# Kernel tuning notes

Measured on AMD Instinct MI355X. Metric: run time of the kernel, lower is better.

Reference implementation:

```python
import jax, jax.numpy as jnp
import numpy as np

N = 50000
E = 800000
IN_FEATS = 128
OUT_FEATS = 16
EDGE_FEATS = 1
NUM_HEADS = 8


def setup_inputs() -> dict:
    key = jax.random.key(0)
    ks = jax.random.split(key, 8)

    def xavier(k, shape):
        fan_in, fan_out = shape[-1], shape[-2] if len(shape) > 1 else shape[-1]
        bound = float(np.sqrt(6.0 / (shape[0] + shape[1])))
        return jax.random.uniform(k, shape, jnp.float32, -bound, bound)

    h = jax.random.normal(ks[0], (N, IN_FEATS), jnp.float32)
    edge_index = jax.random.randint(ks[1], (2, E), 0, N, jnp.int32)
    edge_feat = jax.random.normal(ks[2], (E, EDGE_FEATS), jnp.float32)
    # W_node stored as [in_feats, out_feats*num_heads] so h @ W_node == torch Linear(h)
    W_node = xavier(ks[3], (IN_FEATS, OUT_FEATS * NUM_HEADS))
    W_edge = xavier(ks[4], (EDGE_FEATS, NUM_HEADS))
    a_src = xavier(ks[5], (NUM_HEADS, OUT_FEATS))
    a_dst = xavier(ks[6], (NUM_HEADS, OUT_FEATS))
    return {"h": h, "edge_index": edge_index, "edge_feat": edge_feat,
            "W_node": W_node, "W_edge": W_edge, "a_src": a_src, "a_dst": a_dst}


def reference(h, edge_index, edge_feat, W_node, W_edge, a_src, a_dst):
    n = h.shape[0]
    src, dst = edge_index[0], edge_index[1]
    # node projection: [N, H, F]
    h_trans = (h @ W_node).reshape(n, NUM_HEADS, OUT_FEATS)
    # edge projection: [E, H]
    e_trans = edge_feat @ W_edge
    src_feat = h_trans[src]  # [E, H, F]
    dst_feat = h_trans[dst]  # [E, H, F]
    attn = (src_feat * a_src).sum(-1) + (dst_feat * a_dst).sum(-1) + e_trans  # [E, H]
    attn = jax.nn.leaky_relu(attn, negative_slope=0.2)
    # segment softmax over edges grouped by dst
    max_val = jax.ops.segment_max(attn, dst, num_segments=n)  # [N, H]
    exp_attn = jnp.exp(attn - max_val[dst])
    sum_exp = jax.ops.segment_sum(exp_attn, dst, num_segments=n)  # [N, H]
    alpha = exp_attn / jnp.maximum(sum_exp[dst], 1e-12)  # [E, H]
    msg = src_feat * alpha[..., None]  # [E, H, F]
    out = jax.ops.segment_sum(msg, dst, num_segments=n)  # [N, H, F]
    return out.mean(axis=1)  # [N, F]
```

## Files before the change

### kernel.cpp

```cpp
#include <hip/hip_runtime.h>

#define N_NODES 50000
#define N_EDGES 800000
#define IN_F    128
#define HEADS   8
#define OUT_F   16

typedef unsigned short u16;
typedef __attribute__((ext_vector_type(8))) short bf16x8;
typedef __attribute__((ext_vector_type(4))) float f32x4;

__device__ __forceinline__ float bf2f(u16 u) {
    return __uint_as_float(((unsigned)u) << 16);
}
__device__ __forceinline__ u16 f2bf(float f) {
    unsigned u = __float_as_uint(f);
    unsigned r = 0x7fffu + ((u >> 16) & 1u);
    return (u16)((u + r) >> 16);
}
__device__ __forceinline__ float ldf(const void* p, int i, bool bf) {
    return bf ? bf2f(((const u16*)p)[i]) : ((const float*)p)[i];
}

__global__ void probe_dtype(const void* __restrict__ h, int* __restrict__ flag) {
    if (threadIdx.x == 0 && blockIdx.x == 0) {
        const u16* u = (const u16*)h;
        int cnt = 0;
        for (int i = 0; i < 128; ++i) {
            int e = (u[i] >> 7) & 0xFF;
            if (e >= 90 && e <= 141) cnt++;
        }
        *flag = (cnt >= 110) ? 1 : 0;
    }
}

__global__ __launch_bounds__(256) void init_bufs(float* __restrict__ sum_exp,
                                                 float* __restrict__ out_acc) {
    int i = blockIdx.x * 256 + threadIdx.x;
    if (i < N_NODES * HEADS)  sum_exp[i] = 0.0f;
    if (i < N_NODES * OUT_F)  out_acc[i] = 0.0f;
}

#define WT_STRIDE 136
__global__ __launch_bounds__(256) void node_proj_mfma(
    const void* __restrict__ h, const void* __restrict__ Wn,
    const void* __restrict__ a_srcp, const void* __restrict__ a_dstp,
    const int* __restrict__ flag,
    u16* __restrict__ ht, float* __restrict__ s_src, float* __restrict__ s_dst)
{
    const bool bf = (*flag) != 0;
    __shared__ u16 Wsh[IN_F * WT_STRIDE];
    const int tid = threadIdx.x;

    for (int i = tid; i < IN_F * IN_F; i += 256) {
        int k = i >> 7, c = i & 127;
        u16 v = bf ? ((const u16*)Wn)[i] : f2bf(((const float*)Wn)[i]);
        Wsh[c * WT_STRIDE + k] = v;
    }
    __syncthreads();

    const int wave = tid >> 6, lane = tid & 63;
    const int m = lane & 15, q = lane >> 4;
    const int row_t = blockIdx.x * 64 + wave * 16;

    bf16x8 afr[4];
    int arow = row_t + m;
    if (arow >= N_NODES) arow = N_NODES - 1;
    if (bf) {
        const u16* hp = (const u16*)h + (size_t)arow * IN_F;
        #pragma unroll
        for (int kt = 0; kt < 4; ++kt)
            afr[kt] = *(const bf16x8*)(hp + kt * 32 + q * 8);
    } else {
        const float* hp = (const float*)h + (size_t)arow * IN_F;
        #pragma unroll
        for (int kt = 0; kt < 4; ++kt) {
            bf16x8 t;
            #pragma unroll
            for (int j = 0; j < 8; ++j) t[j] = (short)f2bf(hp[kt * 32 + q * 8 + j]);
            afr[kt] = t;
        }
    }

    for (int ct = 0; ct < 8; ++ct) {
        f32x4 acc = {0.f, 0.f, 0.f, 0.f};
        #pragma unroll
        for (int kt = 0; kt < 4; ++kt) {
            bf16x8 bfr = *(const bf16x8*)(Wsh + (ct * 16 + m) * WT_STRIDE + kt * 32 + q * 8);
            acc = __builtin_amdgcn_mfma_f32_16x16x32_bf16(afr[kt], bfr, acc, 0, 0, 0);
        }
        const float asv = ldf(a_srcp, ct * 16 + m, bf);
        const float adv = ldf(a_dstp, ct * 16 + m, bf);
        float v1[4], v2[4];
        #pragma unroll
        for (int r = 0; r < 4; ++r) {
            int grow = row_t + q * 4 + r;
            if (grow < N_NODES)
                ht[(size_t)grow * IN_F + ct * 16 + m] = f2bf(acc[r]);
            v1[r] = acc[r] * asv;
            v2[r] = acc[r] * adv;
        }
        #pragma unroll
        for (int o = 1; o < 16; o <<= 1) {
            #pragma unroll
            for (int r = 0; r < 4; ++r) {
                v1[r] += __shfl_xor(v1[r], o, 16);
                v2[r] += __shfl_xor(v2[r], o, 16);
            }
        }
        if (m == 0) {
            #pragma unroll
            for (int r = 0; r < 4; ++r) {
                int grow = row_t + q * 4 + r;
                if (grow < N_NODES) {
                    s_src[grow * HEADS + ct] = v1[r];
                    s_dst[grow * HEADS + ct] = v2[r];
                }
            }
        }
    }
}

__device__ __forceinline__ float edge_attn(const int* ei, const void* ef,
                                           const void* We,
                                           const float* s_src, const float* s_dst,
                                           int e, int hh, bool bf,
                                           int& src, int& dst) {
    src = ei[e];
    dst = ei[N_EDGES + e];
    float a = s_src[src * HEADS + hh] + s_dst[dst * HEADS + hh]
            + ldf(ef, e, bf) * ldf(We, hh, bf);
    return (a > 0.0f) ? a : 0.2f * a;
}

__global__ __launch_bounds__(256) void edge_sum(
    const int* __restrict__ ei, const void* __restrict__ ef,
    const void* __restrict__ We, const int* __restrict__ flag,
    const float* __restrict__ s_src, const float* __restrict__ s_dst,
    float* __restrict__ sum_exp)
{
    const bool bf = (*flag) != 0;
    int t = blockIdx.x * 256 + threadIdx.x;
    if (t >= N_EDGES * HEADS) return;
    int e = t >> 3, hh = t & 7, src, dst;
    float a = edge_attn(ei, ef, We, s_src, s_dst, e, hh, bf, src, dst);
    atomicAdd(&sum_exp[dst * HEADS + hh], __expf(a));
}

__global__ __launch_bounds__(256) void edge_aggregate(
    const int* __restrict__ ei, const void* __restrict__ ef,
    const void* __restrict__ We, const int* __restrict__ flag,
    const float* __restrict__ s_src, const float* __restrict__ s_dst,
    const float* __restrict__ sum_exp,
    const u16* __restrict__ ht, float* __restrict__ out_acc)
{
    const bool bf = (*flag) != 0;
    int t = blockIdx.x * 256 + threadIdx.x;
    int e = t >> 4;
    if (e >= N_EDGES) return;
    int lane = threadIdx.x & 15;
    int hh = lane & 7, src, dst;
    float a = edge_attn(ei, ef, We, s_src, s_dst, e, hh, bf, src, dst);
    float alpha = __expf(a) / fmaxf(sum_exp[dst * HEADS + hh], 1e-12f);

    const u16* hp = ht + (size_t)src * IN_F + lane;
    float acc = 0.0f;
    #pragma unroll
    for (int h2 = 0; h2 < HEADS; ++h2) {
        float ah = __shfl(alpha, h2, 16);
        acc = fmaf(ah, bf2f(hp[h2 * 16]), acc);
    }
    atomicAdd(&out_acc[dst * OUT_F + lane], acc * 0.125f);
}

__global__ __launch_bounds__(256) void finalize(const float* __restrict__ out_acc,
                                                void* __restrict__ out,
                                                const int* __restrict__ flag) {
    const bool bf = (*flag) != 0;
    int i = blockIdx.x * 256 + threadIdx.x;
    if (i < N_NODES * OUT_F) {
        float v = out_acc[i];
        if (bf) ((u16*)out)[i] = f2bf(v);
        else    ((float*)out)[i] = v;
    }
}

extern "C" void kernel_launch(void* const* d_in, const int* in_sizes, int n_in,
                              void* d_out, int out_size, void* d_ws, size_t ws_size,
                              hipStream_t stream) {
    const void* h     = d_in[0];
    const int*  ei    = (const int*)d_in[1];
    const void* efeat = d_in[2];
    const void* Wn    = d_in[3];
    const void* We    = d_in[4];
    const void* a_src = d_in[5];
    const void* a_dst = d_in[6];

    char* ws = (char*)d_ws;
    int*   flag    = (int*)ws;   ws += 256;
    u16*   ht      = (u16*)ws;   ws += (size_t)N_NODES * IN_F * 2;
    float* s_src   = (float*)ws; ws += (size_t)N_NODES * HEADS * 4;
    float* s_dst   = (float*)ws; ws += (size_t)N_NODES * HEADS * 4;
    float* sum_exp = (float*)ws; ws += (size_t)N_NODES * HEADS * 4;
    float* out_acc = (float*)ws; ws += (size_t)N_NODES * OUT_F * 4;

    hipLaunchKernelGGL(probe_dtype, dim3(1), dim3(64), 0, stream, h, flag);
    hipLaunchKernelGGL(init_bufs, dim3((N_NODES * OUT_F + 255) / 256), dim3(256),
                       0, stream, sum_exp, out_acc);
    hipLaunchKernelGGL(node_proj_mfma, dim3((N_NODES + 63) / 64), dim3(256),
                       0, stream, h, Wn, a_src, a_dst, flag, ht, s_src, s_dst);
    hipLaunchKernelGGL(edge_sum, dim3((N_EDGES * HEADS + 255) / 256), dim3(256),
                       0, stream, ei, efeat, We, flag, s_src, s_dst, sum_exp);
    hipLaunchKernelGGL(edge_aggregate, dim3((N_EDGES * 16 + 255) / 256), dim3(256),
                       0, stream, ei, efeat, We, flag, s_src, s_dst, sum_exp,
                       ht, out_acc);
    hipLaunchKernelGGL(finalize, dim3((N_NODES * OUT_F + 255) / 256), dim3(256),
                       0, stream, out_acc, d_out, flag);
}
```

Measured before the change: 225.7 us.

## Replace atomic edge softmax with CSR-by-destination segmented aggregation

Builds a CSR grouping of edges by destination (histogram, single-block scan, atomic scatter of src and edge features), then runs one 16-lane group per node. Each group computes the softmax weights, normalises them and accumulates messages in registers, with no max subtraction, which matches the earlier code. This removes the float atomics on sum_exp and out_acc, the second pass over edges and the finalize kernel. In exchange it adds a serial single-block scan, a scatter pass, load imbalance from per-node degree loops, and an edge order within each node that depends on the order of the scatter atomics.

```diff
diff --git a/kernel.cpp b/kernel.cpp
--- a/kernel.cpp
+++ b/kernel.cpp
@@ -34,11 +34,9 @@
     }
 }
 
-__global__ __launch_bounds__(256) void init_bufs(float* __restrict__ sum_exp,
-                                                 float* __restrict__ out_acc) {
+__global__ __launch_bounds__(256) void zero_counts(int* __restrict__ counts) {
     int i = blockIdx.x * 256 + threadIdx.x;
-    if (i < N_NODES * HEADS)  sum_exp[i] = 0.0f;
-    if (i < N_NODES * OUT_F)  out_acc[i] = 0.0f;
+    if (i < N_NODES) counts[i] = 0;
 }
 
 #define WT_STRIDE 136
@@ -121,67 +119,125 @@
     }
 }
 
-__device__ __forceinline__ float edge_attn(const int* ei, const void* ef,
-                                           const void* We,
-                                           const float* s_src, const float* s_dst,
-                                           int e, int hh, bool bf,
-                                           int& src, int& dst) {
-    src = ei[e];
-    dst = ei[N_EDGES + e];
-    float a = s_src[src * HEADS + hh] + s_dst[dst * HEADS + hh]
-            + ldf(ef, e, bf) * ldf(We, hh, bf);
-    return (a > 0.0f) ? a : 0.2f * a;
-}
-
-__global__ __launch_bounds__(256) void edge_sum(
+__global__ __launch_bounds__(256) void hist_dst(const int* __restrict__ ei,
+                                                int* __restrict__ counts) {
+    int t = blockIdx.x * 256 + threadIdx.x;
+    if (t < N_EDGES) atomicAdd(&counts[ei[N_EDGES + t]], 1);
+}
+
+#define SCAN_T 1024
+#define SCAN_C 49
+__global__ __launch_bounds__(SCAN_T) void scan_offsets(
+    const int* __restrict__ counts,
+    int* __restrict__ seg_off, int* __restrict__ cursor)
+{
+    __shared__ int partial[SCAN_T];
+    const int t = threadIdx.x;
+    const int base = t * SCAN_C;
+    int s = 0;
+    for (int j = 0; j < SCAN_C; ++j) {
+        int i = base + j;
+        if (i < N_NODES) s += counts[i];
+    }
+    partial[t] = s;
+    __syncthreads();
+    for (int o = 1; o < SCAN_T; o <<= 1) {
+        int v = (t >= o) ? partial[t - o] : 0;
+        __syncthreads();
+        if (t >= o) partial[t] += v;
+        __syncthreads();
+    }
+    int run = (t > 0) ? partial[t - 1] : 0;
+    for (int j = 0; j < SCAN_C; ++j) {
+        int i = base + j;
+        if (i < N_NODES) {
+            seg_off[i] = run;
+            cursor[i]  = run;
+            run += counts[i];
+        }
+    }
+}
+
+__global__ __launch_bounds__(256) void scatter_edges(
     const int* __restrict__ ei, const void* __restrict__ ef,
+    const int* __restrict__ flag, int* __restrict__ cursor,
+    int* __restrict__ src_s, float* __restrict__ ef_s)
+{
+    const bool bf = (*flag) != 0;
+    int t = blockIdx.x * 256 + threadIdx.x;
+    if (t >= N_EDGES) return;
+    int s = ei[t], d = ei[N_EDGES + t];
+    int pos = atomicAdd(&cursor[d], 1);
+    src_s[pos] = s;
+    ef_s[pos]  = ldf(ef, t, bf);
+}
+
+__global__ __launch_bounds__(256) void aggregate(
+    const int* __restrict__ seg_off, const int* __restrict__ counts,
+    const int* __restrict__ src_s, const float* __restrict__ ef_s,
     const void* __restrict__ We, const int* __restrict__ flag,
     const float* __restrict__ s_src, const float* __restrict__ s_dst,
-    float* __restrict__ sum_exp)
+    const u16* __restrict__ ht, void* __restrict__ out)
 {
     const bool bf = (*flag) != 0;
-    int t = blockIdx.x * 256 + threadIdx.x;
-    if (t >= N_EDGES * HEADS) return;
-    int e = t >> 3, hh = t & 7, src, dst;
-    float a = edge_attn(ei, ef, We, s_src, s_dst, e, hh, bf, src, dst);
-    atomicAdd(&sum_exp[dst * HEADS + hh], __expf(a));
-}
-
-__global__ __launch_bounds__(256) void edge_aggregate(
-    const int* __restrict__ ei, const void* __restrict__ ef,
-    const void* __restrict__ We, const int* __restrict__ flag,
-    const float* __restrict__ s_src, const float* __restrict__ s_dst,
-    const float* __restrict__ sum_exp,
-    const u16* __restrict__ ht, float* __restrict__ out_acc)
-{
-    const bool bf = (*flag) != 0;
-    int t = blockIdx.x * 256 + threadIdx.x;
-    int e = t >> 4;
-    if (e >= N_EDGES) return;
-    int lane = threadIdx.x & 15;
-    int hh = lane & 7, src, dst;
-    float a = edge_attn(ei, ef, We, s_src, s_dst, e, hh, bf, src, dst);
-    float alpha = __expf(a) / fmaxf(sum_exp[dst * HEADS + hh], 1e-12f);
-
-    const u16* hp = ht + (size_t)src * IN_F + lane;
-    float acc = 0.0f;
+    int g = (blockIdx.x * 256 + threadIdx.x) >> 4;
+    if (g >= N_NODES) return;
+    const int lane = threadIdx.x & 15;
+    const int myh  = lane >> 1;
+
+    const int off = seg_off[g];
+    const int deg = counts[g];
+
+    float sdv = 0.0f, wev = 0.0f;
+    if (lane < 8) {
+        sdv = s_dst[g * HEADS + lane];
+        wev = ldf(We, lane, bf);
+    }
+
+    float acc[8];
     #pragma unroll
-    for (int h2 = 0; h2 < HEADS; ++h2) {
-        float ah = __shfl(alpha, h2, 16);
-        acc = fmaf(ah, bf2f(hp[h2 * 16]), acc);
-    }
-    atomicAdd(&out_acc[dst * OUT_F + lane], acc * 0.125f);
-}
-
-__global__ __launch_bounds__(256) void finalize(const float* __restrict__ out_acc,
-                                                void* __restrict__ out,
-                                                const int* __restrict__ flag) {
-    const bool bf = (*flag) != 0;
-    int i = blockIdx.x * 256 + threadIdx.x;
-    if (i < N_NODES * OUT_F) {
-        float v = out_acc[i];
-        if (bf) ((u16*)out)[i] = f2bf(v);
-        else    ((float*)out)[i] = v;
+    for (int j = 0; j < 8; ++j) acc[j] = 0.0f;
+    float sw = 0.0f;
+
+    for (int i = 0; i < deg; ++i) {
+        int src = src_s[off + i];
+        float w = 0.0f;
+        if (lane < 8) {
+            float a = s_src[src * HEADS + lane] + sdv + ef_s[off + i] * wev;
+            a = (a > 0.0f) ? a : 0.2f * a;
+            w = __expf(a);
+        }
+        float wv = __shfl(w, myh, 16);
+        bf16x8 v8 = *(const bf16x8*)(ht + (size_t)src * IN_F + lane * 8);
+        #pragma unroll
+        for (int j = 0; j < 8; ++j)
+            acc[j] = fmaf(wv, bf2f((u16)v8[j]), acc[j]);
+        sw += wv;
+    }
+
+    const float inv = 1.0f / fmaxf(sw, 1e-12f);
+    #pragma unroll
+    for (int j = 0; j < 8; ++j) acc[j] *= inv;
+
+    #pragma unroll
+    for (int o = 2; o < 16; o <<= 1) {
+        #pragma unroll
+        for (int j = 0; j < 8; ++j)
+            acc[j] += __shfl_xor(acc[j], o, 16);
+    }
+
+    if (lane < 2) {
+        if (bf) {
+            u16* op = (u16*)out + g * OUT_F + lane * 8;
+            bf16x8 o8;
+            #pragma unroll
+            for (int j = 0; j < 8; ++j) o8[j] = (short)f2bf(acc[j] * 0.125f);
+            *(bf16x8*)op = o8;
+        } else {
+            float* op = (float*)out + g * OUT_F + lane * 8;
+            #pragma unroll
+            for (int j = 0; j < 8; ++j) op[j] = acc[j] * 0.125f;
+        }
     }
 }
 
@@ -201,19 +257,24 @@
     u16*   ht      = (u16*)ws;   ws += (size_t)N_NODES * IN_F * 2;
     float* s_src   = (float*)ws; ws += (size_t)N_NODES * HEADS * 4;
     float* s_dst   = (float*)ws; ws += (size_t)N_NODES * HEADS * 4;
-    float* sum_exp = (float*)ws; ws += (size_t)N_NODES * HEADS * 4;
-    float* out_acc = (float*)ws; ws += (size_t)N_NODES * OUT_F * 4;
+    int*   counts  = (int*)ws;   ws += (size_t)N_NODES * 4;
+    int*   seg_off = (int*)ws;   ws += (size_t)N_NODES * 4;
+    int*   cursor  = (int*)ws;   ws += (size_t)N_NODES * 4;
+    int*   src_s   = (int*)ws;   ws += (size_t)N_EDGES * 4;
+    float* ef_s    = (float*)ws; ws += (size_t)N_EDGES * 4;
 
     hipLaunchKernelGGL(probe_dtype, dim3(1), dim3(64), 0, stream, h, flag);
-    hipLaunchKernelGGL(init_bufs, dim3((N_NODES * OUT_F + 255) / 256), dim3(256),
-                       0, stream, sum_exp, out_acc);
+    hipLaunchKernelGGL(zero_counts, dim3((N_NODES + 255) / 256), dim3(256),
+                       0, stream, counts);
     hipLaunchKernelGGL(node_proj_mfma, dim3((N_NODES + 63) / 64), dim3(256),
                        0, stream, h, Wn, a_src, a_dst, flag, ht, s_src, s_dst);
-    hipLaunchKernelGGL(edge_sum, dim3((N_EDGES * HEADS + 255) / 256), dim3(256),
-                       0, stream, ei, efeat, We, flag, s_src, s_dst, sum_exp);
-    hipLaunchKernelGGL(edge_aggregate, dim3((N_EDGES * 16 + 255) / 256), dim3(256),
-                       0, stream, ei, efeat, We, flag, s_src, s_dst, sum_exp,
-                       ht, out_acc);
-    hipLaunchKernelGGL(finalize, dim3((N_NODES * OUT_F + 255) / 256), dim3(256),
-                       0, stream, out_acc, d_out, flag);
-}
+    hipLaunchKernelGGL(hist_dst, dim3((N_EDGES + 255) / 256), dim3(256),
+                       0, stream, ei, counts);
+    hipLaunchKernelGGL(scan_offsets, dim3(1), dim3(SCAN_T), 0, stream,
+                       counts, seg_off, cursor);
+    hipLaunchKernelGGL(scatter_edges, dim3((N_EDGES + 255) / 256), dim3(256),
+                       0, stream, ei, efeat, flag, cursor, src_s, ef_s);
+    hipLaunchKernelGGL(aggregate, dim3((N_NODES * 16 + 255) / 256), dim3(256),
+                       0, stream, seg_off, counts, src_s, ef_s, We, flag,
+                       s_src, s_dst, ht, d_out);
+}
```

Result: slower. 382.8 us (+69.6%).
